# Optimization experiments

Hardware: AMD Instinct MI355X
Metric: run time of the kernel (lower is better)

Reference implementation:

```python
import jax, jax.numpy as jnp
import numpy as np

B, NSYS, D, H, L = 16, 1024, 256, 4, 2
DH = D // H
DFF = 4 * D
EPS_UPD = 0.1    # eps=0.1 on update LayerNorms in the source
EPS_SYS = 1e-5   # default LayerNorm eps for sys_norm


def _ln(x, g, b, eps):
    mu = jnp.mean(x, axis=-1, keepdims=True)
    var = jnp.var(x, axis=-1, keepdims=True)
    return (x - mu) * jax.lax.rsqrt(var + eps) * g + b


def _hitr(q, k, mask, Wq, Wk, Wv, Wo, W1, W2, in_g, in_b, out_g, out_b):
    # HierarchicalTransformer block: masked multi-head cross-attention + FFN
    Bq, Nq, _ = q.shape
    Nk = k.shape[1]
    Q = (q @ Wq).reshape(Bq, Nq, H, DH)
    K = (k @ Wk).reshape(Bq, Nk, H, DH)
    V = (k @ Wv).reshape(Bq, Nk, H, DH)
    scores = jnp.einsum('bqhd,bkhd->bhqk', Q, K) / jnp.sqrt(jnp.float32(DH))
    scores = jnp.where(mask[None, None] > 0, scores, jnp.float32(-1e9))
    attn = jax.nn.softmax(scores, axis=-1)
    ctx = jnp.einsum('bhqk,bkhd->bqhd', attn, V).reshape(Bq, Nq, D)
    x = _ln(q + ctx @ Wo, in_g, in_b, EPS_UPD)
    ffn = jax.nn.gelu(x @ W1) @ W2
    return _ln(x + ffn, out_g, out_b, EPS_UPD)


def setup_inputs() -> dict:
    key = jax.random.key(0)
    ks = jax.random.split(key, 16)
    s = jnp.float32(0.02)
    return {
        'system_embedding': jax.random.normal(ks[0], (B, NSYS, D), jnp.float32),
        'update_tensor': jnp.zeros((B, NSYS, D), jnp.float32),
        'sys_table': jax.random.normal(ks[1], (NSYS + 1, D), jnp.float32) * s,
        'Wq': jax.random.normal(ks[2], (L, D, D), jnp.float32) * s,
        'Wk': jax.random.normal(ks[3], (L, D, D), jnp.float32) * s,
        'Wv': jax.random.normal(ks[4], (L, D, D), jnp.float32) * s,
        'Wo': jax.random.normal(ks[5], (L, D, D), jnp.float32) * s,
        'W1': jax.random.normal(ks[6], (L, D, DFF), jnp.float32) * s,
        'W2': jax.random.normal(ks[7], (L, DFF, D), jnp.float32) * s,
        'sys_g': jnp.ones((D,), jnp.float32),
        'sys_b': jnp.zeros((D,), jnp.float32),
        'in_g': jnp.ones((D,), jnp.float32),
        'in_b': jnp.zeros((D,), jnp.float32),
        'out_g': jnp.ones((D,), jnp.float32),
        'out_b': jnp.zeros((D,), jnp.float32),
        'query_idx': jax.random.randint(ks[8], (L, NSYS), 0, NSYS, jnp.int32),
        'key_idx': jax.random.randint(ks[9], (L, NSYS), 0, NSYS, jnp.int32),
        'mask': jax.random.randint(ks[10], (L, NSYS, NSYS), 0, 2, jnp.int32),
    }


def reference(system_embedding, update_tensor, sys_table, Wq, Wk, Wv, Wo, W1, W2,
              sys_g, sys_b, in_g, in_b, out_g, out_b, query_idx, key_idx, mask):
    # get_sys2sys, with_indices=True path: per hierarchy level, gather node
    # embeddings + accumulated effects, masked cross-attention, accumulate.
    upd = update_tensor
    for l in range(L):  # fixed, small hierarchy depth
        qi, ki = query_idx[l], key_idx[l]
        q_emb = sys_table[qi]          # [NSYS, D], shared across batch
        k_emb = sys_table[ki]
        q_eff = upd[:, qi, :]          # per-batch gather of accumulated effects
        k_eff = upd[:, ki, :]
        q = _ln(q_emb[None] + q_eff, sys_g, sys_b, EPS_SYS)
        k = _ln(k_emb[None] + k_eff, sys_g, sys_b, EPS_SYS)
        hitr = _hitr(q, k, mask[l], Wq[l], Wk[l], Wv[l], Wo[l], W1[l], W2[l],
                     in_g, in_b, out_g, out_b)
        upd = upd + hitr               # scatter-back accumulation
    return system_embedding + upd
```

## Files before the change

### kernel.cpp

```cpp
#include <hip/hip_runtime.h>
#include <stdint.h>

#define NSYS 1024
#define DD   256
#define HH   4
#define DHH  64
#define DFFN 1024
#define NL   2
#define BBATCH 16
#define NTOK (BBATCH * NSYS)

typedef unsigned short u16;
typedef unsigned int   u32;
typedef unsigned long long u64;
typedef __bf16 bf16x8 __attribute__((ext_vector_type(8)));
typedef float  f32x4  __attribute__((ext_vector_type(4)));

__device__ __forceinline__ float b2f(u16 u) {
    union { u32 i; float f; } x; x.i = ((u32)u) << 16; return x.f;
}
__device__ __forceinline__ u16 f2b(float f) {
    union { float f; u32 i; } x; x.f = f;
    u32 r = (x.i + 0x7fffu + ((x.i >> 16) & 1u)) >> 16;
    return (u16)r;
}
__device__ __forceinline__ float ld_in(const void* p, size_t i, int f32mode) {
    return f32mode ? ((const float*)p)[i] : b2f(((const u16*)p)[i]);
}
__device__ __forceinline__ float wave_sum64(float v) {
#pragma unroll
    for (int o = 32; o >= 1; o >>= 1) v += __shfl_xor(v, o);
    return v;
}
__device__ __forceinline__ float red_sum16(float v) {
#pragma unroll
    for (int o = 1; o < 16; o <<= 1) v += __shfl_xor(v, o);
    return v;
}
__device__ __forceinline__ void gload_lds16(const u16* g, u16* l) {
    __builtin_amdgcn_global_load_lds(
        (const __attribute__((address_space(1))) u32*)g,
        (__attribute__((address_space(3))) u32*)l, 16, 0, 0);
}

__global__ __launch_bounds__(256) void k_prep(
    const void* sys_g, const void* sys_b, const void* in_g, const void* in_b,
    const void* out_g, const void* out_b, const void* table,
    const void* Wq, const void* Wk, const void* Wv, const void* Wo_,
    const void* W1, const void* W2, const void* upd_in, const int* __restrict__ mask,
    u16* __restrict__ Wtqkv, u16* __restrict__ Wto, u16* __restrict__ Wt1,
    u16* __restrict__ Wt2c, u16* __restrict__ tabc, u16* __restrict__ vecs,
    u64* __restrict__ mbits, float* __restrict__ upd)
{
    const int f = (((const u32*)sys_g)[0] == 0x3F800000u) ? 1 : 0;
    const int blk = blockIdx.x, tid = threadIdx.x;
    if (blk < 2048) {
        int idx = blk * 256 + tid;
        int mat = idx >> 16, within = idx & 65535;
        int layer = mat >> 2, which = mat & 3;
        const void* srcs[4] = { Wq, Wk, Wv, Wo_ };
        float v = ld_in(srcs[which], (size_t)layer * 65536 + within, f);
        int r = within >> 8, c = within & 255;
        u16* dst = (which < 3) ? (Wtqkv + ((size_t)layer * 3 + which) * 65536)
                               : (Wto + (size_t)layer * 65536);
        dst[c * 256 + r] = f2b(v);
    } else if (blk < 4096) {
        int idx = (blk - 2048) * 256 + tid;
        int layer = idx >> 18, within = idx & 262143;
        int r = within >> 10, c = within & 1023;
        Wt1[(size_t)layer * 262144 + c * 256 + r] = f2b(ld_in(W1, idx, f));
    } else if (blk < 6144) {
        int idx = (blk - 4096) * 256 + tid;
        int layer = idx >> 18, within = idx & 262143;
        int k = within >> 8, n = within & 255;
        int chunk = k >> 9, kin = k & 511;
        Wt2c[(size_t)layer * 262144 + chunk * 131072 + n * 512 + kin] = f2b(ld_in(W2, idx, f));
    } else if (blk < 7169) {
        int i = (blk - 6144) * 256 + tid;
        tabc[i] = f2b(ld_in(table, i, f));
    } else if (blk == 7169) {
        const void* ps[6] = { sys_g, sys_b, in_g, in_b, out_g, out_b };
#pragma unroll
        for (int j = 0; j < 6; ++j)
            vecs[j * 256 + tid] = f2b(ld_in(ps[j], tid, f));
    } else if (blk < 15362) {
        int word = (blk - 7170) * 4 + (tid >> 6);
        int lane = tid & 63;
        u64 m = __ballot(mask[(size_t)word * 64 + lane] > 0);
        if (lane == 0) mbits[word] = m;
    } else {
        int i = (blk - 15362) * 256 + tid;
        upd[i] = ld_in(upd_in, i, f);
    }
}

__global__ __launch_bounds__(256) void k_gather_ln(
    const u16* __restrict__ table, const float* __restrict__ upd,
    const int* __restrict__ qidx, const int* __restrict__ kidx,
    const u16* __restrict__ g, const u16* __restrict__ bias,
    u16* __restrict__ qout, u16* __restrict__ kout)
{
    const int grow = blockIdx.x * 4 + (threadIdx.x >> 6);
    const int b = grow >> 10;
    const int n = grow & (NSYS - 1);
    const int t = threadIdx.x & 63;
    ushort4 gv = *(const ushort4*)(g + t * 4);
    ushort4 bv = *(const ushort4*)(bias + t * 4);
    float gg[4] = { b2f(gv.x), b2f(gv.y), b2f(gv.z), b2f(gv.w) };
    float bb[4] = { b2f(bv.x), b2f(bv.y), b2f(bv.z), b2f(bv.w) };
#pragma unroll
    for (int pass = 0; pass < 2; ++pass) {
        const int idx = (pass ? kidx : qidx)[n];
        ushort4 tv = *(const ushort4*)(table + (size_t)idx * DD + t * 4);
        float4  uv = *(const float4*)(upd + ((size_t)b * NSYS + idx) * DD + t * 4);
        float v[4] = { b2f(tv.x) + uv.x, b2f(tv.y) + uv.y, b2f(tv.z) + uv.z, b2f(tv.w) + uv.w };
        float s = wave_sum64(v[0] + v[1] + v[2] + v[3]);
        float mean = s * (1.f / 256.f);
        float q = 0.f;
#pragma unroll
        for (int j = 0; j < 4; ++j) { float d = v[j] - mean; q += d * d; }
        q = wave_sum64(q);
        float rs = rsqrtf(q * (1.f / 256.f) + 1e-5f);
        ushort4 o;
        o.x = f2b((v[0] - mean) * rs * gg[0] + bb[0]);
        o.y = f2b((v[1] - mean) * rs * gg[1] + bb[1]);
        o.z = f2b((v[2] - mean) * rs * gg[2] + bb[2]);
        o.w = f2b((v[3] - mean) * rs * gg[3] + bb[3]);
        u16* op = (pass ? kout : qout) + (size_t)grow * DD + t * 4;
        *(ushort4*)op = o;
    }
}

template<int MODE>
__device__ __forceinline__ void gemm_core(
    const u16* __restrict__ A, const u16* __restrict__ Bt, void* __restrict__ Cv,
    int M, int N, int K, int bx, int by)
{
    __shared__ u16 As[128 * 32];
    __shared__ u16 Bs[128 * 32];
    const int tid = threadIdx.x, lane = tid & 63, wv = tid >> 6;
    const int wy = wv >> 1, wx = wv & 1, quad = lane >> 4, l15 = lane & 15;
    const int row0 = bx * 128, col0 = by * 128;
    const int r0w = wv * 32;
    const int lrow = lane >> 2;
    const int lcol = (lane & 3) * 8;
    const f32x4 zero4 = { 0.f, 0.f, 0.f, 0.f };
    f32x4 acc[4][4];
#pragma unroll
    for (int i = 0; i < 4; ++i)
#pragma unroll
        for (int j = 0; j < 4; ++j) acc[i][j] = zero4;

    for (int k0 = 0; k0 < K; k0 += 32) {
#pragma unroll
        for (int s = 0; s < 2; ++s) {
            const int rr = r0w + s * 16;
            gload_lds16(A  + (size_t)(row0 + rr + lrow) * K + k0 + lcol, &As[rr * 32]);
            gload_lds16(Bt + (size_t)(col0 + rr + lrow) * K + k0 + lcol, &Bs[rr * 32]);
        }
        __syncthreads();
        bf16x8 af[4], bfv[4];
#pragma unroll
        for (int i = 0; i < 4; ++i) af[i]  = *(const bf16x8*)&As[(wy * 64 + i * 16 + l15) * 32 + quad * 8];
#pragma unroll
        for (int j = 0; j < 4; ++j) bfv[j] = *(const bf16x8*)&Bs[(wx * 64 + j * 16 + l15) * 32 + quad * 8];
#pragma unroll
        for (int i = 0; i < 4; ++i)
#pragma unroll
            for (int j = 0; j < 4; ++j)
                acc[i][j] = __builtin_amdgcn_mfma_f32_16x16x32_bf16(af[i], bfv[j], acc[i][j], 0, 0, 0);
        __syncthreads();
    }
#pragma unroll
    for (int i = 0; i < 4; ++i)
#pragma unroll
        for (int j = 0; j < 4; ++j)
#pragma unroll
            for (int r = 0; r < 4; ++r) {
                int row = row0 + wy * 64 + i * 16 + quad * 4 + r;
                int col = col0 + wx * 64 + j * 16 + l15;
                float v = acc[i][j][r];
                if (MODE == 1) {
                    float u = 1.5957691216057308f * (v + 0.044715f * v * v * v);
                    v = v * __builtin_amdgcn_rcpf(1.f + __expf(-u));
                }
                if (MODE <= 1) {
                    ((u16*)Cv)[(size_t)row * N + col] = f2b(v);
                } else if (MODE == 2) {
                    ((float*)Cv)[(size_t)row * N + col] = v;
                } else {
                    ((float*)Cv)[(size_t)row * N + col] += v;
                }
            }
}

template<int MODE>
__global__ __launch_bounds__(256) void k_gemm(
    const u16* __restrict__ A, const u16* __restrict__ Bt, void* __restrict__ C,
    int M, int N, int K)
{
    gemm_core<MODE>(A, Bt, C, M, N, K, blockIdx.x, blockIdx.y);
}

__global__ __launch_bounds__(256) void k_gemm_qkv(
    const u16* __restrict__ qb, const u16* __restrict__ kb,
    const u16* __restrict__ Wt3, u16* __restrict__ outbase)
{
    const int z = blockIdx.z;
    const u16* A  = (z == 0) ? qb : kb;
    const u16* Bt = Wt3 + (size_t)z * (DD * DD);
    const int zslot = (z == 0) ? 0 : ((z == 1) ? 2 : 1);
    u16* C = outbase + (size_t)zslot * ((size_t)NTOK * DD);
    gemm_core<0>(A, Bt, C, NTOK, DD, DD, blockIdx.x, blockIdx.y);
}

__global__ __launch_bounds__(256) void k_attn(
    const u16* __restrict__ Qb, const u16* __restrict__ Kb, const u16* __restrict__ Vb,
    const u64* __restrict__ mbits, u16* __restrict__ ctx)
{
    __shared__ u16 Ks[64][72];
    __shared__ u16 Vs[64][72];
    __shared__ u16 Ps[4][16][72];

    const int tid = threadIdx.x, lane = tid & 63, w = tid >> 6;
    const int quad = lane >> 4, l15 = lane & 15;
    const int bid = blockIdx.x;
    const int g = bid & 63, qt = bid >> 6;
    const int h = g & 3, b = g >> 2;
    const int q0 = qt * 64;
    const size_t base = ((size_t)b * NSYS) * DD + h * DHH;
    const int row_w = q0 + w * 16;

    for (int c = lane; c < 128; c += 64) {
        int r = c >> 3, c8 = (c & 7) << 3;
        *(uint4*)&Ps[w][r][c8] = *(const uint4*)(Qb + base + (size_t)(row_w + r) * DD + c8);
    }
    asm volatile("s_waitcnt lgkmcnt(0)" ::: "memory");
    bf16x8 qf[2];
#pragma unroll
    for (int kx = 0; kx < 2; ++kx)
        qf[kx] = *(const bf16x8*)&Ps[w][l15][kx * 32 + quad * 8];

    float l_r[4] = { 0.f, 0.f, 0.f, 0.f };
    const f32x4 zero4 = { 0.f, 0.f, 0.f, 0.f };
    f32x4 O[4];
#pragma unroll
    for (int j = 0; j < 4; ++j) O[j] = zero4;

    const u16* Kp = Kb + base;
    const u16* Vp = Vb + base;
    uint4 kreg[2]; ushort4 vreg[4];
#pragma unroll
    for (int s = 0; s < 2; ++s) {
        int c = tid + (s << 8);
        int r = c >> 3, c8 = (c & 7) << 3;
        kreg[s] = *(const uint4*)(Kp + (size_t)r * DD + c8);
    }
#pragma unroll
    for (int s = 0; s < 4; ++s) {
        int c = tid + (s << 8);
        int key = c >> 4, d0 = (c & 15) << 2;
        vreg[s] = *(const ushort4*)(Vp + (size_t)key * DD + d0);
    }

    for (int kv0 = 0; kv0 < NSYS; kv0 += 64) {
        __syncthreads();
#pragma unroll
        for (int s = 0; s < 2; ++s) {
            int c = tid + (s << 8);
            int r = c >> 3, c8 = (c & 7) << 3;
            *(uint4*)&Ks[r][c8] = kreg[s];
        }
#pragma unroll
        for (int s = 0; s < 4; ++s) {
            int c = tid + (s << 8);
            int key = c >> 4, d0 = (c & 15) << 2;
            Vs[d0 + 0][key] = vreg[s].x; Vs[d0 + 1][key] = vreg[s].y;
            Vs[d0 + 2][key] = vreg[s].z; Vs[d0 + 3][key] = vreg[s].w;
        }
        __syncthreads();

        if (kv0 + 64 < NSYS) {
            const int nkv = kv0 + 64;
#pragma unroll
            for (int s = 0; s < 2; ++s) {
                int c = tid + (s << 8);
                int r = c >> 3, c8 = (c & 7) << 3;
                kreg[s] = *(const uint4*)(Kp + (size_t)(nkv + r) * DD + c8);
            }
#pragma unroll
            for (int s = 0; s < 4; ++s) {
                int c = tid + (s << 8);
                int key = c >> 4, d0 = (c & 15) << 2;
                vreg[s] = *(const ushort4*)(Vp + (size_t)(nkv + key) * DD + d0);
            }
        }

        u64 mw[4];
#pragma unroll
        for (int r = 0; r < 4; ++r)
            mw[r] = mbits[(size_t)(row_w + quad * 4 + r) * 16 + (kv0 >> 6)];

        f32x4 S[4];
#pragma unroll
        for (int j = 0; j < 4; ++j) S[j] = zero4;
#pragma unroll
        for (int kx = 0; kx < 2; ++kx)
#pragma unroll
            for (int j = 0; j < 4; ++j) {
                bf16x8 bfv = *(const bf16x8*)&Ks[j * 16 + l15][kx * 32 + quad * 8];
                S[j] = __builtin_amdgcn_mfma_f32_16x16x32_bf16(qf[kx], bfv, S[j], 0, 0, 0);
            }

#pragma unroll
        for (int r = 0; r < 4; ++r)
#pragma unroll
            for (int j = 0; j < 4; ++j) {
                float e = __expf(S[j][r] * 0.125f);
                bool keep = (mw[r] >> (j * 16 + l15)) & 1ull;
                float p = keep ? e : 0.f;
                l_r[r] += p;
                Ps[w][quad * 4 + r][j * 16 + l15] = f2b(p);
            }
        asm volatile("s_waitcnt lgkmcnt(0)" ::: "memory");

#pragma unroll
        for (int kx = 0; kx < 2; ++kx) {
            bf16x8 af = *(const bf16x8*)&Ps[w][l15][kx * 32 + quad * 8];
#pragma unroll
            for (int j = 0; j < 4; ++j) {
                bf16x8 bfv = *(const bf16x8*)&Vs[j * 16 + l15][kx * 32 + quad * 8];
                O[j] = __builtin_amdgcn_mfma_f32_16x16x32_bf16(af, bfv, O[j], 0, 0, 0);
            }
        }
    }

#pragma unroll
    for (int r = 0; r < 4; ++r) {
        float lt = red_sum16(l_r[r]);
        float li = 1.f / lt;
        int row = row_w + quad * 4 + r;
#pragma unroll
        for (int j = 0; j < 4; ++j) {
            int col = h * DHH + j * 16 + l15;
            ctx[((size_t)b * NSYS + row) * DD + col] = f2b(O[j][r] * li);
        }
    }
}

__global__ __launch_bounds__(256) void k_ln_add(
    const u16* __restrict__ a, const u16* __restrict__ c,
    const u16* __restrict__ g, const u16* __restrict__ bias,
    float eps, u16* __restrict__ out)
{
    const int row = blockIdx.x * 4 + (threadIdx.x >> 6);
    const int t = threadIdx.x & 63;
    ushort4 av = *(const ushort4*)(a + (size_t)row * DD + t * 4);
    ushort4 cv = *(const ushort4*)(c + (size_t)row * DD + t * 4);
    float v[4] = { b2f(av.x) + b2f(cv.x), b2f(av.y) + b2f(cv.y),
                   b2f(av.z) + b2f(cv.z), b2f(av.w) + b2f(cv.w) };
    float s = wave_sum64(v[0] + v[1] + v[2] + v[3]);
    float mean = s * (1.f / 256.f);
    float q = 0.f;
#pragma unroll
    for (int j = 0; j < 4; ++j) { float d = v[j] - mean; q += d * d; }
    q = wave_sum64(q);
    float rs = rsqrtf(q * (1.f / 256.f) + eps);
    ushort4 gv = *(const ushort4*)(g + t * 4);
    ushort4 bv = *(const ushort4*)(bias + t * 4);
    ushort4 o;
    o.x = f2b((v[0] - mean) * rs * b2f(gv.x) + b2f(bv.x));
    o.y = f2b((v[1] - mean) * rs * b2f(gv.y) + b2f(bv.y));
    o.z = f2b((v[2] - mean) * rs * b2f(gv.z) + b2f(bv.z));
    o.w = f2b((v[3] - mean) * rs * b2f(gv.w) + b2f(bv.w));
    *(ushort4*)(out + (size_t)row * DD + t * 4) = o;
}

__global__ __launch_bounds__(256) void k_ln_acc(
    const u16* __restrict__ a, const float* __restrict__ c,
    const u16* __restrict__ g, const u16* __restrict__ bias,
    float eps, float* __restrict__ upd)
{
    const int row = blockIdx.x * 4 + (threadIdx.x >> 6);
    const int t = threadIdx.x & 63;
    ushort4 av = *(const ushort4*)(a + (size_t)row * DD + t * 4);
    float4  cv = *(const float4*)(c + (size_t)row * DD + t * 4);
    float v[4] = { b2f(av.x) + cv.x, b2f(av.y) + cv.y,
                   b2f(av.z) + cv.z, b2f(av.w) + cv.w };
    float s = wave_sum64(v[0] + v[1] + v[2] + v[3]);
    float mean = s * (1.f / 256.f);
    float q = 0.f;
#pragma unroll
    for (int j = 0; j < 4; ++j) { float d = v[j] - mean; q += d * d; }
    q = wave_sum64(q);
    float rs = rsqrtf(q * (1.f / 256.f) + eps);
    ushort4 gv = *(const ushort4*)(g + t * 4);
    ushort4 bv = *(const ushort4*)(bias + t * 4);
    float* up = upd + (size_t)row * DD + t * 4;
    float4 u = *(float4*)up;
    u.x += (v[0] - mean) * rs * b2f(gv.x) + b2f(bv.x);
    u.y += (v[1] - mean) * rs * b2f(gv.y) + b2f(bv.y);
    u.z += (v[2] - mean) * rs * b2f(gv.z) + b2f(bv.z);
    u.w += (v[3] - mean) * rs * b2f(gv.w) + b2f(bv.w);
    *(float4*)up = u;
}

__global__ void k_out(const void* __restrict__ sys, const float* __restrict__ upd,
                      void* __restrict__ out, int n, const void* __restrict__ sys_g) {
    const int f = (((const u32*)sys_g)[0] == 0x3F800000u) ? 1 : 0;
    int i = blockIdx.x * 256 + threadIdx.x;
    if (i < n) {
        float v = ld_in(sys, i, f) + upd[i];
        if (f) ((float*)out)[i] = v;
        else   ((u16*)out)[i]   = f2b(v);
    }
}

extern "C" void kernel_launch(void* const* d_in, const int* in_sizes, int n_in,
                              void* d_out, int out_size, void* d_ws, size_t ws_size,
                              hipStream_t stream)
{
    const void* sys_emb = d_in[0];
    const void* upd_in  = d_in[1];
    const void* table   = d_in[2];
    const void* Wq = d_in[3];
    const void* Wk = d_in[4];
    const void* Wv = d_in[5];
    const void* Wo = d_in[6];
    const void* W1 = d_in[7];
    const void* W2 = d_in[8];
    const void* sys_g = d_in[9];
    const void* sys_b = d_in[10];
    const void* in_g  = d_in[11];
    const void* in_b  = d_in[12];
    const void* out_g = d_in[13];
    const void* out_b = d_in[14];
    const int* qidx = (const int*)d_in[15];
    const int* kidx = (const int*)d_in[16];
    const int* mask = (const int*)d_in[17];

    char* ws = (char*)d_ws;
    float* upd = (float*)(ws + 0);
    u16* qb    = (u16*)(ws + 16777216);
    u16* kb    = (u16*)(ws + 25165824);
    u16* Qb    = (u16*)(ws + 33554432);
    u16* Vb    = (u16*)(ws + 41943040);
    u16* Kb    = (u16*)(ws + 50331648);
    u16* Wtqkv = (u16*)(ws + 58720256);
    u16* Wto   = (u16*)(ws + 59506688);
    u16* Wt1   = (u16*)(ws + 59768832);
    u16* Wt2c  = (u16*)(ws + 60817408);
    u16* tabc  = (u16*)(ws + 61865984);
    u16* vecs  = (u16*)(ws + 62390784);
    u64* mbits = (u64*)(ws + 62394368);
    u16*  ctxb = kb;
    u16*  tb   = Qb;
    u16*  xb   = Kb;
    u16*  hc   = qb;
    float* facc = (float*)(ws + 33554432);
    const u16* c_sys_g = vecs + 0 * 256;
    const u16* c_sys_b = vecs + 1 * 256;
    const u16* c_in_g  = vecs + 2 * 256;
    const u16* c_in_b  = vecs + 3 * 256;
    const u16* c_out_g = vecs + 4 * 256;
    const u16* c_out_b = vecs + 5 * 256;

    k_prep<<<31746, 256, 0, stream>>>(sys_g, sys_b, in_g, in_b, out_g, out_b, table,
                                      Wq, Wk, Wv, Wo, W1, W2, upd_in, mask,
                                      Wtqkv, Wto, Wt1, Wt2c, tabc, vecs, mbits, upd);

    const dim3 gP(NTOK / 128, DD / 128);
    for (int l = 0; l < NL; ++l) {
        k_gather_ln<<<NTOK / 4, 256, 0, stream>>>(tabc, upd, qidx + l * NSYS, kidx + l * NSYS,
                                                  c_sys_g, c_sys_b, qb, kb);
        k_gemm_qkv<<<dim3(NTOK / 128, DD / 128, 3), 256, 0, stream>>>(
            qb, kb, Wtqkv + (size_t)l * 3 * 65536, Qb);
        k_attn<<<1024, 256, 0, stream>>>(
            Qb, Kb, Vb, mbits + (size_t)l * 16384, ctxb);
        k_gemm<0><<<gP, 256, 0, stream>>>(ctxb, Wto + (size_t)l * 65536, tb, NTOK, DD, DD);
        k_ln_add<<<NTOK / 4, 256, 0, stream>>>(qb, tb, c_in_g, c_in_b, 0.1f, xb);
        for (int c = 0; c < 2; ++c) {
            k_gemm<1><<<dim3(NTOK / 128, 4), 256, 0, stream>>>(
                xb, Wt1 + (size_t)l * 262144 + (size_t)c * 131072, hc, NTOK, 512, DD);
            if (c == 0)
                k_gemm<2><<<gP, 256, 0, stream>>>(
                    hc, Wt2c + (size_t)l * 262144 + (size_t)c * 131072, facc, NTOK, DD, 512);
            else
                k_gemm<3><<<gP, 256, 0, stream>>>(
                    hc, Wt2c + (size_t)l * 262144 + (size_t)c * 131072, facc, NTOK, DD, 512);
        }
        k_ln_acc<<<NTOK / 4, 256, 0, stream>>>(xb, facc, c_out_g, c_out_b, 0.1f, upd);
    }
    k_out<<<NTOK * DD / 256, 256, 0, stream>>>(sys_emb, upd, d_out, NTOK * DD, sys_g);
}
```

Baseline: 513.9 us.

## Double-buffer K/V tiles in attention kernel to drop one barrier per tile

Gives the attention kernel two LDS buffers for the K and V tiles. Each iteration now writes the next tile into the spare buffer after its MFMAs and prefetches the tile after that, so only one __syncthreads is needed per tile instead of two. It also replaces the hand-written round-to-nearest-even bf16 conversion with the compiler's native __bf16 cast. The cost is twice the LDS for K and V, which may lower occupancy, and the LDS stores now sit at the end of the loop body rather than overlapping the barrier.

Result: slower. 578.6 us (+12.6%).

```diff
diff --git a/kernel.cpp b/kernel.cpp
--- a/kernel.cpp
+++ b/kernel.cpp
@@ -20,9 +20,7 @@
     union { u32 i; float f; } x; x.i = ((u32)u) << 16; return x.f;
 }
 __device__ __forceinline__ u16 f2b(float f) {
-    union { float f; u32 i; } x; x.f = f;
-    u32 r = (x.i + 0x7fffu + ((x.i >> 16) & 1u)) >> 16;
-    return (u16)r;
+    union { __bf16 h; u16 u; } cv; cv.h = (__bf16)f; return cv.u;
 }
 __device__ __forceinline__ float ld_in(const void* p, size_t i, int f32mode) {
     return f32mode ? ((const float*)p)[i] : b2f(((const u16*)p)[i]);
@@ -218,8 +216,8 @@
     const u16* __restrict__ Qb, const u16* __restrict__ Kb, const u16* __restrict__ Vb,
     const u64* __restrict__ mbits, u16* __restrict__ ctx)
 {
-    __shared__ u16 Ks[64][72];
-    __shared__ u16 Vs[64][72];
+    __shared__ u16 Ks[2][64][72];
+    __shared__ u16 Vs[2][64][72];
     __shared__ u16 Ps[4][16][72];
 
     const int tid = threadIdx.x, lane = tid & 63, w = tid >> 6;
@@ -250,56 +248,48 @@
     const u16* Kp = Kb + base;
     const u16* Vp = Vb + base;
     uint4 kreg[2]; ushort4 vreg[4];
+
 #pragma unroll
     for (int s = 0; s < 2; ++s) {
         int c = tid + (s << 8);
-        int r = c >> 3, c8 = (c & 7) << 3;
-        kreg[s] = *(const uint4*)(Kp + (size_t)r * DD + c8);
+        kreg[s] = *(const uint4*)(Kp + (size_t)(c >> 3) * DD + ((c & 7) << 3));
+    }
+#pragma unroll
+    for (int s = 0; s < 4; ++s) {
+        int c = tid + (s << 8);
+        vreg[s] = *(const ushort4*)(Vp + (size_t)(c >> 4) * DD + ((c & 15) << 2));
+    }
+#pragma unroll
+    for (int s = 0; s < 2; ++s) {
+        int c = tid + (s << 8);
+        *(uint4*)&Ks[0][c >> 3][(c & 7) << 3] = kreg[s];
     }
 #pragma unroll
     for (int s = 0; s < 4; ++s) {
         int c = tid + (s << 8);
         int key = c >> 4, d0 = (c & 15) << 2;
-        vreg[s] = *(const ushort4*)(Vp + (size_t)key * DD + d0);
-    }
-
-    for (int kv0 = 0; kv0 < NSYS; kv0 += 64) {
+        Vs[0][d0 + 0][key] = vreg[s].x; Vs[0][d0 + 1][key] = vreg[s].y;
+        Vs[0][d0 + 2][key] = vreg[s].z; Vs[0][d0 + 3][key] = vreg[s].w;
+    }
+#pragma unroll
+    for (int s = 0; s < 2; ++s) {
+        int c = tid + (s << 8);
+        kreg[s] = *(const uint4*)(Kp + (size_t)(64 + (c >> 3)) * DD + ((c & 7) << 3));
+    }
+#pragma unroll
+    for (int s = 0; s < 4; ++s) {
+        int c = tid + (s << 8);
+        vreg[s] = *(const ushort4*)(Vp + (size_t)(64 + (c >> 4)) * DD + ((c & 15) << 2));
+    }
+
+    for (int it = 0; it < 16; ++it) {
+        const int buf = it & 1;
         __syncthreads();
-#pragma unroll
-        for (int s = 0; s < 2; ++s) {
-            int c = tid + (s << 8);
-            int r = c >> 3, c8 = (c & 7) << 3;
-            *(uint4*)&Ks[r][c8] = kreg[s];
-        }
-#pragma unroll
-        for (int s = 0; s < 4; ++s) {
-            int c = tid + (s << 8);
-            int key = c >> 4, d0 = (c & 15) << 2;
-            Vs[d0 + 0][key] = vreg[s].x; Vs[d0 + 1][key] = vreg[s].y;
-            Vs[d0 + 2][key] = vreg[s].z; Vs[d0 + 3][key] = vreg[s].w;
-        }
-        __syncthreads();
-
-        if (kv0 + 64 < NSYS) {
-            const int nkv = kv0 + 64;
-#pragma unroll
-            for (int s = 0; s < 2; ++s) {
-                int c = tid + (s << 8);
-                int r = c >> 3, c8 = (c & 7) << 3;
-                kreg[s] = *(const uint4*)(Kp + (size_t)(nkv + r) * DD + c8);
-            }
-#pragma unroll
-            for (int s = 0; s < 4; ++s) {
-                int c = tid + (s << 8);
-                int key = c >> 4, d0 = (c & 15) << 2;
-                vreg[s] = *(const ushort4*)(Vp + (size_t)(nkv + key) * DD + d0);
-            }
-        }
 
         u64 mw[4];
 #pragma unroll
         for (int r = 0; r < 4; ++r)
-            mw[r] = mbits[(size_t)(row_w + quad * 4 + r) * 16 + (kv0 >> 6)];
+            mw[r] = mbits[(size_t)(row_w + quad * 4 + r) * 16 + it];
 
         f32x4 S[4];
 #pragma unroll
@@ -308,7 +298,7 @@
         for (int kx = 0; kx < 2; ++kx)
 #pragma unroll
             for (int j = 0; j < 4; ++j) {
-                bf16x8 bfv = *(const bf16x8*)&Ks[j * 16 + l15][kx * 32 + quad * 8];
+                bf16x8 bfv = *(const bf16x8*)&Ks[buf][j * 16 + l15][kx * 32 + quad * 8];
                 S[j] = __builtin_amdgcn_mfma_f32_16x16x32_bf16(qf[kx], bfv, S[j], 0, 0, 0);
             }
 
@@ -329,8 +319,36 @@
             bf16x8 af = *(const bf16x8*)&Ps[w][l15][kx * 32 + quad * 8];
 #pragma unroll
             for (int j = 0; j < 4; ++j) {
-                bf16x8 bfv = *(const bf16x8*)&Vs[j * 16 + l15][kx * 32 + quad * 8];
+                bf16x8 bfv = *(const bf16x8*)&Vs[buf][j * 16 + l15][kx * 32 + quad * 8];
                 O[j] = __builtin_amdgcn_mfma_f32_16x16x32_bf16(af, bfv, O[j], 0, 0, 0);
+            }
+        }
+
+        if (it + 1 < 16) {
+#pragma unroll
+            for (int s = 0; s < 2; ++s) {
+                int c = tid + (s << 8);
+                *(uint4*)&Ks[buf ^ 1][c >> 3][(c & 7) << 3] = kreg[s];
+            }
+#pragma unroll
+            for (int s = 0; s < 4; ++s) {
+                int c = tid + (s << 8);
+                int key = c >> 4, d0 = (c & 15) << 2;
+                Vs[buf ^ 1][d0 + 0][key] = vreg[s].x; Vs[buf ^ 1][d0 + 1][key] = vreg[s].y;
+                Vs[buf ^ 1][d0 + 2][key] = vreg[s].z; Vs[buf ^ 1][d0 + 3][key] = vreg[s].w;
+            }
+            if (it + 2 < 16) {
+                const int nkv = (it + 2) * 64;
+#pragma unroll
+                for (int s = 0; s < 2; ++s) {
+                    int c = tid + (s << 8);
+                    kreg[s] = *(const uint4*)(Kp + (size_t)(nkv + (c >> 3)) * DD + ((c & 7) << 3));
+                }
+#pragma unroll
+                for (int s = 0; s < 4; ++s) {
+                    int c = tid + (s << 8);
+                    vreg[s] = *(const ushort4*)(Vp + (size_t)(nkv + (c >> 4)) * DD + ((c & 15) << 2));
+                }
             }
         }
     }
```

## Split attention KV range in two with a combine kernel for more blocks

Applied to the files above, without the earlier changes.

Attention is split across the key dimension into two halves, which doubles the grid to 2048 blocks. Each half writes an unnormalized partial output in bf16 along with its row sums. A new combine kernel adds the two partials and normalizes them. The aim is better occupancy across the CUs, at the cost of extra memory traffic, an extra launch, and bf16 rounding of the unnormalized partials. The float-to-bf16 conversion also now uses the native __bf16 cast.

After: 532.8 us. 3.7% more time.

```diff
diff --git a/kernel.cpp b/kernel.cpp
--- a/kernel.cpp
+++ b/kernel.cpp
@@ -20,9 +20,7 @@
     union { u32 i; float f; } x; x.i = ((u32)u) << 16; return x.f;
 }
 __device__ __forceinline__ u16 f2b(float f) {
-    union { float f; u32 i; } x; x.f = f;
-    u32 r = (x.i + 0x7fffu + ((x.i >> 16) & 1u)) >> 16;
-    return (u16)r;
+    union { __bf16 h; u16 u; } cv; cv.h = (__bf16)f; return cv.u;
 }
 __device__ __forceinline__ float ld_in(const void* p, size_t i, int f32mode) {
     return f32mode ? ((const float*)p)[i] : b2f(((const u16*)p)[i]);
@@ -216,7 +214,7 @@
 
 __global__ __launch_bounds__(256) void k_attn(
     const u16* __restrict__ Qb, const u16* __restrict__ Kb, const u16* __restrict__ Vb,
-    const u64* __restrict__ mbits, u16* __restrict__ ctx)
+    const u64* __restrict__ mbits, u16* __restrict__ Opart, float* __restrict__ lpart)
 {
     __shared__ u16 Ks[64][72];
     __shared__ u16 Vs[64][72];
@@ -225,11 +223,12 @@
     const int tid = threadIdx.x, lane = tid & 63, w = tid >> 6;
     const int quad = lane >> 4, l15 = lane & 15;
     const int bid = blockIdx.x;
-    const int g = bid & 63, qt = bid >> 6;
+    const int g = bid & 63, qt = (bid >> 6) & 15, split = bid >> 10;
     const int h = g & 3, b = g >> 2;
     const int q0 = qt * 64;
     const size_t base = ((size_t)b * NSYS) * DD + h * DHH;
     const int row_w = q0 + w * 16;
+    const int kv_base = split * 512;
 
     for (int c = lane; c < 128; c += 64) {
         int r = c >> 3, c8 = (c & 7) << 3;
@@ -253,23 +252,20 @@
 #pragma unroll
     for (int s = 0; s < 2; ++s) {
         int c = tid + (s << 8);
-        int r = c >> 3, c8 = (c & 7) << 3;
-        kreg[s] = *(const uint4*)(Kp + (size_t)r * DD + c8);
+        kreg[s] = *(const uint4*)(Kp + (size_t)(kv_base + (c >> 3)) * DD + ((c & 7) << 3));
     }
 #pragma unroll
     for (int s = 0; s < 4; ++s) {
         int c = tid + (s << 8);
-        int key = c >> 4, d0 = (c & 15) << 2;
-        vreg[s] = *(const ushort4*)(Vp + (size_t)key * DD + d0);
-    }
-
-    for (int kv0 = 0; kv0 < NSYS; kv0 += 64) {
+        vreg[s] = *(const ushort4*)(Vp + (size_t)(kv_base + (c >> 4)) * DD + ((c & 15) << 2));
+    }
+
+    for (int it = 0; it < 8; ++it) {
         __syncthreads();
 #pragma unroll
         for (int s = 0; s < 2; ++s) {
             int c = tid + (s << 8);
-            int r = c >> 3, c8 = (c & 7) << 3;
-            *(uint4*)&Ks[r][c8] = kreg[s];
+            *(uint4*)&Ks[c >> 3][(c & 7) << 3] = kreg[s];
         }
 #pragma unroll
         for (int s = 0; s < 4; ++s) {
@@ -280,26 +276,24 @@
         }
         __syncthreads();
 
-        if (kv0 + 64 < NSYS) {
-            const int nkv = kv0 + 64;
+        if (it + 1 < 8) {
+            const int nkv = kv_base + (it + 1) * 64;
 #pragma unroll
             for (int s = 0; s < 2; ++s) {
                 int c = tid + (s << 8);
-                int r = c >> 3, c8 = (c & 7) << 3;
-                kreg[s] = *(const uint4*)(Kp + (size_t)(nkv + r) * DD + c8);
+                kreg[s] = *(const uint4*)(Kp + (size_t)(nkv + (c >> 3)) * DD + ((c & 7) << 3));
             }
 #pragma unroll
             for (int s = 0; s < 4; ++s) {
                 int c = tid + (s << 8);
-                int key = c >> 4, d0 = (c & 15) << 2;
-                vreg[s] = *(const ushort4*)(Vp + (size_t)(nkv + key) * DD + d0);
+                vreg[s] = *(const ushort4*)(Vp + (size_t)(nkv + (c >> 4)) * DD + ((c & 15) << 2));
             }
         }
 
         u64 mw[4];
 #pragma unroll
         for (int r = 0; r < 4; ++r)
-            mw[r] = mbits[(size_t)(row_w + quad * 4 + r) * 16 + (kv0 >> 6)];
+            mw[r] = mbits[(size_t)(row_w + quad * 4 + r) * 16 + split * 8 + it];
 
         f32x4 S[4];
 #pragma unroll
@@ -338,14 +332,35 @@
 #pragma unroll
     for (int r = 0; r < 4; ++r) {
         float lt = red_sum16(l_r[r]);
-        float li = 1.f / lt;
         int row = row_w + quad * 4 + r;
+        size_t grow = (size_t)b * NSYS + row;
+        if (l15 == 0)
+            lpart[((size_t)split * NTOK + grow) * HH + h] = lt;
 #pragma unroll
         for (int j = 0; j < 4; ++j) {
             int col = h * DHH + j * 16 + l15;
-            ctx[((size_t)b * NSYS + row) * DD + col] = f2b(O[j][r] * li);
-        }
-    }
+            Opart[(size_t)split * NTOK * DD + grow * DD + col] = f2b(O[j][r]);
+        }
+    }
+}
+
+__global__ __launch_bounds__(256) void k_attn_combine(
+    const u16* __restrict__ Opart, const float* __restrict__ lpart, u16* __restrict__ ctx)
+{
+    const int grow = blockIdx.x * 4 + (threadIdx.x >> 6);
+    const int t = threadIdx.x & 63;
+    const int head = t >> 4;
+    float l0 = lpart[(size_t)grow * HH + head];
+    float l1 = lpart[((size_t)NTOK + grow) * HH + head];
+    float inv = 1.f / (l0 + l1);
+    ushort4 a = *(const ushort4*)(Opart + (size_t)grow * DD + t * 4);
+    ushort4 c = *(const ushort4*)(Opart + (size_t)NTOK * DD + (size_t)grow * DD + t * 4);
+    ushort4 o;
+    o.x = f2b((b2f(a.x) + b2f(c.x)) * inv);
+    o.y = f2b((b2f(a.y) + b2f(c.y)) * inv);
+    o.z = f2b((b2f(a.z) + b2f(c.z)) * inv);
+    o.w = f2b((b2f(a.w) + b2f(c.w)) * inv);
+    *(ushort4*)(ctx + (size_t)grow * DD + t * 4) = o;
 }
 
 __global__ __launch_bounds__(256) void k_ln_add(
@@ -453,6 +468,8 @@
     u16* tabc  = (u16*)(ws + 61865984);
     u16* vecs  = (u16*)(ws + 62390784);
     u64* mbits = (u64*)(ws + 62394368);
+    u16* Opart = (u16*)(ws + 62656512);
+    float* lpart = (float*)(ws + 79433728);
     u16*  ctxb = kb;
     u16*  tb   = Qb;
     u16*  xb   = Kb;
@@ -475,8 +492,9 @@
                                                   c_sys_g, c_sys_b, qb, kb);
         k_gemm_qkv<<<dim3(NTOK / 128, DD / 128, 3), 256, 0, stream>>>(
             qb, kb, Wtqkv + (size_t)l * 3 * 65536, Qb);
-        k_attn<<<1024, 256, 0, stream>>>(
-            Qb, Kb, Vb, mbits + (size_t)l * 16384, ctxb);
+        k_attn<<<2048, 256, 0, stream>>>(
+            Qb, Kb, Vb, mbits + (size_t)l * 16384, Opart, lpart);
+        k_attn_combine<<<NTOK / 4, 256, 0, stream>>>(Opart, lpart, ctxb);
         k_gemm<0><<<gP, 256, 0, stream>>>(ctxb, Wto + (size_t)l * 65536, tb, NTOK, DD, DD);
         k_ln_add<<<NTOK / 4, 256, 0, stream>>>(qb, tb, c_in_g, c_in_b, 0.1f, xb);
         for (int c = 0; c < 2; ++c) {
```

## Split-K the N=256 GEMMs into two partials and fuse final output add

Applied to the files above, without the earlier changes.

The Wo and W2 GEMMs (N=256, only 256 blocks) now split K in two along blockIdx.z, doubling the grid to 512 blocks, and write fp32 partials that the following LayerNorm kernels sum. The last layer's LayerNorm-accumulate is fused with the final system_embedding add, which removes the separate k_out pass. The Wo output also changes from a bf16 intermediate to fp32 partials, and f2b now uses the native bf16 conversion. Occupancy on the many-CU device should improve, at the cost of extra fp32 partial traffic of about 32MB per GEMM.

Result: no change. 510.0 us (median of 2 runs) (-0.8%).

```diff
diff --git a/kernel.cpp b/kernel.cpp
--- a/kernel.cpp
+++ b/kernel.cpp
@@ -20,9 +20,7 @@
     union { u32 i; float f; } x; x.i = ((u32)u) << 16; return x.f;
 }
 __device__ __forceinline__ u16 f2b(float f) {
-    union { float f; u32 i; } x; x.f = f;
-    u32 r = (x.i + 0x7fffu + ((x.i >> 16) & 1u)) >> 16;
-    return (u16)r;
+    union { __bf16 h; u16 u; } cv; cv.h = (__bf16)f; return cv.u;
 }
 __device__ __forceinline__ float ld_in(const void* p, size_t i, int f32mode) {
     return f32mode ? ((const float*)p)[i] : b2f(((const u16*)p)[i]);
@@ -134,7 +132,7 @@
 template<int MODE>
 __device__ __forceinline__ void gemm_core(
     const u16* __restrict__ A, const u16* __restrict__ Bt, void* __restrict__ Cv,
-    int M, int N, int K, int bx, int by)
+    int M, int N, int Kfull, int koff, int klen, int bx, int by)
 {
     __shared__ u16 As[128 * 32];
     __shared__ u16 Bs[128 * 32];
@@ -151,12 +149,12 @@
 #pragma unroll
         for (int j = 0; j < 4; ++j) acc[i][j] = zero4;
 
-    for (int k0 = 0; k0 < K; k0 += 32) {
+    for (int k0 = koff; k0 < koff + klen; k0 += 32) {
 #pragma unroll
         for (int s = 0; s < 2; ++s) {
             const int rr = r0w + s * 16;
-            gload_lds16(A  + (size_t)(row0 + rr + lrow) * K + k0 + lcol, &As[rr * 32]);
-            gload_lds16(Bt + (size_t)(col0 + rr + lrow) * K + k0 + lcol, &Bs[rr * 32]);
+            gload_lds16(A  + (size_t)(row0 + rr + lrow) * Kfull + k0 + lcol, &As[rr * 32]);
+            gload_lds16(Bt + (size_t)(col0 + rr + lrow) * Kfull + k0 + lcol, &Bs[rr * 32]);
         }
         __syncthreads();
         bf16x8 af[4], bfv[4];
@@ -199,7 +197,18 @@
     const u16* __restrict__ A, const u16* __restrict__ Bt, void* __restrict__ C,
     int M, int N, int K)
 {
-    gemm_core<MODE>(A, Bt, C, M, N, K, blockIdx.x, blockIdx.y);
+    gemm_core<MODE>(A, Bt, C, M, N, K, 0, K, blockIdx.x, blockIdx.y);
+}
+
+template<int MODE>
+__global__ __launch_bounds__(256) void k_gemm_sk2(
+    const u16* __restrict__ A, const u16* __restrict__ Bt,
+    float* __restrict__ C0, float* __restrict__ C1,
+    int M, int N, int Kfull, int klen)
+{
+    const int z = blockIdx.z;
+    float* Cv = z ? C1 : C0;
+    gemm_core<MODE>(A, Bt, Cv, M, N, Kfull, z * klen, klen, blockIdx.x, blockIdx.y);
 }
 
 __global__ __launch_bounds__(256) void k_gemm_qkv(
@@ -211,7 +220,7 @@
     const u16* Bt = Wt3 + (size_t)z * (DD * DD);
     const int zslot = (z == 0) ? 0 : ((z == 1) ? 2 : 1);
     u16* C = outbase + (size_t)zslot * ((size_t)NTOK * DD);
-    gemm_core<0>(A, Bt, C, NTOK, DD, DD, blockIdx.x, blockIdx.y);
+    gemm_core<0>(A, Bt, C, NTOK, DD, DD, 0, DD, blockIdx.x, blockIdx.y);
 }
 
 __global__ __launch_bounds__(256) void k_attn(
@@ -253,14 +262,12 @@
 #pragma unroll
     for (int s = 0; s < 2; ++s) {
         int c = tid + (s << 8);
-        int r = c >> 3, c8 = (c & 7) << 3;
-        kreg[s] = *(const uint4*)(Kp + (size_t)r * DD + c8);
+        kreg[s] = *(const uint4*)(Kp + (size_t)(c >> 3) * DD + ((c & 7) << 3));
     }
 #pragma unroll
     for (int s = 0; s < 4; ++s) {
         int c = tid + (s << 8);
-        int key = c >> 4, d0 = (c & 15) << 2;
-        vreg[s] = *(const ushort4*)(Vp + (size_t)key * DD + d0);
+        vreg[s] = *(const ushort4*)(Vp + (size_t)(c >> 4) * DD + ((c & 15) << 2));
     }
 
     for (int kv0 = 0; kv0 < NSYS; kv0 += 64) {
@@ -268,8 +275,7 @@
 #pragma unroll
         for (int s = 0; s < 2; ++s) {
             int c = tid + (s << 8);
-            int r = c >> 3, c8 = (c & 7) << 3;
-            *(uint4*)&Ks[r][c8] = kreg[s];
+            *(uint4*)&Ks[c >> 3][(c & 7) << 3] = kreg[s];
         }
 #pragma unroll
         for (int s = 0; s < 4; ++s) {
@@ -285,14 +291,12 @@
 #pragma unroll
             for (int s = 0; s < 2; ++s) {
                 int c = tid + (s << 8);
-                int r = c >> 3, c8 = (c & 7) << 3;
-                kreg[s] = *(const uint4*)(Kp + (size_t)(nkv + r) * DD + c8);
+                kreg[s] = *(const uint4*)(Kp + (size_t)(nkv + (c >> 3)) * DD + ((c & 7) << 3));
             }
 #pragma unroll
             for (int s = 0; s < 4; ++s) {
                 int c = tid + (s << 8);
-                int key = c >> 4, d0 = (c & 15) << 2;
-                vreg[s] = *(const ushort4*)(Vp + (size_t)(nkv + key) * DD + d0);
+                vreg[s] = *(const ushort4*)(Vp + (size_t)(nkv + (c >> 4)) * DD + ((c & 15) << 2));
             }
         }
 
@@ -348,17 +352,18 @@
     }
 }
 
-__global__ __launch_bounds__(256) void k_ln_add(
-    const u16* __restrict__ a, const u16* __restrict__ c,
+__global__ __launch_bounds__(256) void k_ln_add3(
+    const u16* __restrict__ a, const float* __restrict__ c0, const float* __restrict__ c1,
     const u16* __restrict__ g, const u16* __restrict__ bias,
     float eps, u16* __restrict__ out)
 {
     const int row = blockIdx.x * 4 + (threadIdx.x >> 6);
     const int t = threadIdx.x & 63;
     ushort4 av = *(const ushort4*)(a + (size_t)row * DD + t * 4);
-    ushort4 cv = *(const ushort4*)(c + (size_t)row * DD + t * 4);
-    float v[4] = { b2f(av.x) + b2f(cv.x), b2f(av.y) + b2f(cv.y),
-                   b2f(av.z) + b2f(cv.z), b2f(av.w) + b2f(cv.w) };
+    float4  c0v = *(const float4*)(c0 + (size_t)row * DD + t * 4);
+    float4  c1v = *(const float4*)(c1 + (size_t)row * DD + t * 4);
+    float v[4] = { b2f(av.x) + c0v.x + c1v.x, b2f(av.y) + c0v.y + c1v.y,
+                   b2f(av.z) + c0v.z + c1v.z, b2f(av.w) + c0v.w + c1v.w };
     float s = wave_sum64(v[0] + v[1] + v[2] + v[3]);
     float mean = s * (1.f / 256.f);
     float q = 0.f;
@@ -376,17 +381,18 @@
     *(ushort4*)(out + (size_t)row * DD + t * 4) = o;
 }
 
-__global__ __launch_bounds__(256) void k_ln_acc(
-    const u16* __restrict__ a, const float* __restrict__ c,
+__global__ __launch_bounds__(256) void k_ln_acc3(
+    const u16* __restrict__ a, const float* __restrict__ c0, const float* __restrict__ c1,
     const u16* __restrict__ g, const u16* __restrict__ bias,
     float eps, float* __restrict__ upd)
 {
     const int row = blockIdx.x * 4 + (threadIdx.x >> 6);
     const int t = threadIdx.x & 63;
     ushort4 av = *(const ushort4*)(a + (size_t)row * DD + t * 4);
-    float4  cv = *(const float4*)(c + (size_t)row * DD + t * 4);
-    float v[4] = { b2f(av.x) + cv.x, b2f(av.y) + cv.y,
-                   b2f(av.z) + cv.z, b2f(av.w) + cv.w };
+    float4  c0v = *(const float4*)(c0 + (size_t)row * DD + t * 4);
+    float4  c1v = *(const float4*)(c1 + (size_t)row * DD + t * 4);
+    float v[4] = { b2f(av.x) + c0v.x + c1v.x, b2f(av.y) + c0v.y + c1v.y,
+                   b2f(av.z) + c0v.z + c1v.z, b2f(av.w) + c0v.w + c1v.w };
     float s = wave_sum64(v[0] + v[1] + v[2] + v[3]);
     float mean = s * (1.f / 256.f);
     float q = 0.f;
@@ -405,14 +411,46 @@
     *(float4*)up = u;
 }
 
-__global__ void k_out(const void* __restrict__ sys, const float* __restrict__ upd,
-                      void* __restrict__ out, int n, const void* __restrict__ sys_g) {
+__global__ __launch_bounds__(256) void k_ln_acc3_out(
+    const u16* __restrict__ a, const float* __restrict__ c0, const float* __restrict__ c1,
+    const u16* __restrict__ g, const u16* __restrict__ bias,
+    float eps, const float* __restrict__ upd,
+    const void* __restrict__ sys, void* __restrict__ out, const void* __restrict__ sys_g)
+{
     const int f = (((const u32*)sys_g)[0] == 0x3F800000u) ? 1 : 0;
-    int i = blockIdx.x * 256 + threadIdx.x;
-    if (i < n) {
-        float v = ld_in(sys, i, f) + upd[i];
-        if (f) ((float*)out)[i] = v;
-        else   ((u16*)out)[i]   = f2b(v);
+    const int row = blockIdx.x * 4 + (threadIdx.x >> 6);
+    const int t = threadIdx.x & 63;
+    ushort4 av = *(const ushort4*)(a + (size_t)row * DD + t * 4);
+    float4  c0v = *(const float4*)(c0 + (size_t)row * DD + t * 4);
+    float4  c1v = *(const float4*)(c1 + (size_t)row * DD + t * 4);
+    float v[4] = { b2f(av.x) + c0v.x + c1v.x, b2f(av.y) + c0v.y + c1v.y,
+                   b2f(av.z) + c0v.z + c1v.z, b2f(av.w) + c0v.w + c1v.w };
+    float s = wave_sum64(v[0] + v[1] + v[2] + v[3]);
+    float mean = s * (1.f / 256.f);
+    float q = 0.f;
+#pragma unroll
+    for (int j = 0; j < 4; ++j) { float d = v[j] - mean; q += d * d; }
+    q = wave_sum64(q);
+    float rs = rsqrtf(q * (1.f / 256.f) + eps);
+    ushort4 gv = *(const ushort4*)(g + t * 4);
+    ushort4 bv = *(const ushort4*)(bias + t * 4);
+    float4 u = *(const float4*)(upd + (size_t)row * DD + t * 4);
+    float ln0 = (v[0] - mean) * rs * b2f(gv.x) + b2f(bv.x);
+    float ln1 = (v[1] - mean) * rs * b2f(gv.y) + b2f(bv.y);
+    float ln2 = (v[2] - mean) * rs * b2f(gv.z) + b2f(bv.z);
+    float ln3 = (v[3] - mean) * rs * b2f(gv.w) + b2f(bv.w);
+    size_t o0 = (size_t)row * DD + t * 4;
+    float r0 = ld_in(sys, o0 + 0, f) + u.x + ln0;
+    float r1 = ld_in(sys, o0 + 1, f) + u.y + ln1;
+    float r2 = ld_in(sys, o0 + 2, f) + u.z + ln2;
+    float r3 = ld_in(sys, o0 + 3, f) + u.w + ln3;
+    if (f) {
+        float4 o = { r0, r1, r2, r3 };
+        *(float4*)((float*)out + o0) = o;
+    } else {
+        ushort4 o;
+        o.x = f2b(r0); o.y = f2b(r1); o.z = f2b(r2); o.w = f2b(r3);
+        *(ushort4*)((u16*)out + o0) = o;
     }
 }
 
@@ -453,11 +491,11 @@
     u16* tabc  = (u16*)(ws + 61865984);
     u16* vecs  = (u16*)(ws + 62390784);
     u64* mbits = (u64*)(ws + 62394368);
+    float* part0 = (float*)(ws + 33554432);
+    float* part1 = (float*)(ws + 62656512);
     u16*  ctxb = kb;
-    u16*  tb   = Qb;
     u16*  xb   = Kb;
     u16*  hc   = qb;
-    float* facc = (float*)(ws + 33554432);
     const u16* c_sys_g = vecs + 0 * 256;
     const u16* c_sys_b = vecs + 1 * 256;
     const u16* c_in_g  = vecs + 2 * 256;
@@ -469,7 +507,6 @@
                                       Wq, Wk, Wv, Wo, W1, W2, upd_in, mask,
                                       Wtqkv, Wto, Wt1, Wt2c, tabc, vecs, mbits, upd);
 
-    const dim3 gP(NTOK / 128, DD / 128);
     for (int l = 0; l < NL; ++l) {
         k_gather_ln<<<NTOK / 4, 256, 0, stream>>>(tabc, upd, qidx + l * NSYS, kidx + l * NSYS,
                                                   c_sys_g, c_sys_b, qb, kb);
@@ -477,19 +514,25 @@
             qb, kb, Wtqkv + (size_t)l * 3 * 65536, Qb);
         k_attn<<<1024, 256, 0, stream>>>(
             Qb, Kb, Vb, mbits + (size_t)l * 16384, ctxb);
-        k_gemm<0><<<gP, 256, 0, stream>>>(ctxb, Wto + (size_t)l * 65536, tb, NTOK, DD, DD);
-        k_ln_add<<<NTOK / 4, 256, 0, stream>>>(qb, tb, c_in_g, c_in_b, 0.1f, xb);
+        k_gemm_sk2<2><<<dim3(NTOK / 128, DD / 128, 2), 256, 0, stream>>>(
+            ctxb, Wto + (size_t)l * 65536, part0, part1, NTOK, DD, DD, 128);
+        k_ln_add3<<<NTOK / 4, 256, 0, stream>>>(qb, part0, part1, c_in_g, c_in_b, 0.1f, xb);
         for (int c = 0; c < 2; ++c) {
             k_gemm<1><<<dim3(NTOK / 128, 4), 256, 0, stream>>>(
                 xb, Wt1 + (size_t)l * 262144 + (size_t)c * 131072, hc, NTOK, 512, DD);
             if (c == 0)
-                k_gemm<2><<<gP, 256, 0, stream>>>(
-                    hc, Wt2c + (size_t)l * 262144 + (size_t)c * 131072, facc, NTOK, DD, 512);
+                k_gemm_sk2<2><<<dim3(NTOK / 128, DD / 128, 2), 256, 0, stream>>>(
+                    hc, Wt2c + (size_t)l * 262144 + (size_t)c * 131072, part0, part1,
+                    NTOK, DD, 512, 256);
             else
-                k_gemm<3><<<gP, 256, 0, stream>>>(
-                    hc, Wt2c + (size_t)l * 262144 + (size_t)c * 131072, facc, NTOK, DD, 512);
-        }
-        k_ln_acc<<<NTOK / 4, 256, 0, stream>>>(xb, facc, c_out_g, c_out_b, 0.1f, upd);
-    }
-    k_out<<<NTOK * DD / 256, 256, 0, stream>>>(sys_emb, upd, d_out, NTOK * DD, sys_g);
-}
+                k_gemm_sk2<3><<<dim3(NTOK / 128, DD / 128, 2), 256, 0, stream>>>(
+                    hc, Wt2c + (size_t)l * 262144 + (size_t)c * 131072, part0, part1,
+                    NTOK, DD, 512, 256);
+        }
+        if (l == 0)
+            k_ln_acc3<<<NTOK / 4, 256, 0, stream>>>(xb, part0, part1, c_out_g, c_out_b, 0.1f, upd);
+        else
+            k_ln_acc3_out<<<NTOK / 4, 256, 0, stream>>>(xb, part0, part1, c_out_g, c_out_b, 0.1f,
+                                                        upd, sys_emb, d_out, sys_g);
+    }
+}
```
